# Kernel tuning notes

Hardware: AMD Instinct MI355X
Metric: run time of the kernel (lower is better)

The kernel has to match this reference:

```python
import jax, jax.numpy as jnp
import numpy as np

N = 100000
D = 128
E = 1600000


def setup_inputs() -> dict:
    key = jax.random.key(0)
    k1, k2, k3, k4 = jax.random.split(key, 4)
    x = jax.random.normal(k1, (N, D), dtype=jnp.float32)
    edge_index = jax.random.randint(k2, (2, E), 0, N, dtype=jnp.int64)
    edge_weight = jax.random.uniform(k3, (E,), dtype=jnp.float32)
    x0 = jax.random.normal(k4, (N, D), dtype=jnp.float32)
    return {
        "t": jnp.zeros((), dtype=jnp.float32),
        "x": x,
        "edge_index": edge_index,
        "edge_weight": edge_weight,
        "x0": x0,
        "alpha_train": jnp.zeros((), dtype=jnp.float32),
        "beta_train": jnp.zeros((), dtype=jnp.float32),
        "source_train": jnp.zeros((), dtype=jnp.float32),
    }


def reference(t, x, edge_index, edge_weight, x0, alpha_train, beta_train, source_train):
    # sigmoid-gated diffusion/reaction coefficients
    alpha = jax.nn.sigmoid(alpha_train) * 0.1
    beta = jax.nn.sigmoid(beta_train) * 0.1
    # sparse A @ x: out[row] += w * x[col]  (torch_sparse.spmm convention)
    row, col = edge_index[0], edge_index[1]
    msgs = x[col] * edge_weight[:, None]            # [E, D]
    ax = jax.ops.segment_sum(msgs, row, num_segments=N)  # [N, D]
    diffusion = ax - x
    reaction = -(x - 1.0) * x
    f = alpha * diffusion + beta * reaction
    source_term = jnp.clip(source_train * x0, -1.0, 1.0)
    return f + source_term * 0.1
```

## Files before the change

kernel.cpp:

```cpp
#include <hip/hip_runtime.h>
#include <math.h>


#define D_FEAT 128
#define RPB 256
#define NB_MAX 400
#define SORT_CAP 5120
#define EPB 8192

__device__ __forceinline__ float sigmoid_f(float v) {
    return 1.0f / (1.0f + __expf(-v));
}

__global__ void zero_kernel(int* __restrict__ p, int n) {
    int i = blockIdx.x * blockDim.x + threadIdx.x;
    if (i < n) p[i] = 0;
}

__global__ __launch_bounds__(256) void count_kernel(const int* __restrict__ rows,
                                                    int* __restrict__ cnt, int E, int NB) {
    __shared__ int hist[NB_MAX];
    int t = threadIdx.x;
    for (int i = t; i < NB; i += 256) hist[i] = 0;
    __syncthreads();
    int nE4 = E >> 2;
    int base4 = blockIdx.x * (EPB / 4);
#pragma unroll
    for (int k = 0; k < EPB / 4 / 256; ++k) {
        int i4 = base4 + k * 256 + t;
        if (i4 < nE4) {
            int4 r = ((const int4*)rows)[i4];
            atomicAdd(&hist[r.x >> 8], 1);
            atomicAdd(&hist[r.y >> 8], 1);
            atomicAdd(&hist[r.z >> 8], 1);
            atomicAdd(&hist[r.w >> 8], 1);
        }
    }
    if (blockIdx.x == 0 && t < (E & 3))
        atomicAdd(&hist[rows[(nE4 << 2) + t] >> 8], 1);
    __syncthreads();
    for (int i = t; i < NB; i += 256) {
        int c = hist[i];
        if (c) atomicAdd(&cnt[i], c);
    }
}

__global__ void scan_kernel(const int* __restrict__ cnt, int* __restrict__ bstart,
                            int* __restrict__ gcur, int NB) {
    int lane = threadIdx.x;
    int carry = 0;
    for (int base = 0; base < NB; base += 64) {
        int idx = base + lane;
        int v = (idx < NB) ? cnt[idx] : 0;
        int incl = v;
#pragma unroll
        for (int d = 1; d < 64; d <<= 1) {
            int tt = __shfl_up(incl, d);
            if (lane >= d) incl += tt;
        }
        int tot = __shfl(incl, 63);
        int excl = incl - v + carry;
        if (idx < NB) { bstart[idx] = excl; gcur[idx] = excl; }
        carry += tot;
    }
    if (lane == 0) bstart[NB] = carry;
}

__global__ __launch_bounds__(256) void place_kernel(const int* __restrict__ rows,
                                                    const int* __restrict__ cols,
                                                    const float* __restrict__ w,
                                                    const float* __restrict__ alpha_p,
                                                    int* __restrict__ gcur,
                                                    int2* __restrict__ raw, int E, int NB) {
    __shared__ int hist[NB_MAX];
    __shared__ int basep[NB_MAX];
    const float alpha = sigmoid_f(alpha_p[0]) * 0.1f;
    int t = threadIdx.x;
    for (int i = t; i < NB; i += 256) hist[i] = 0;
    __syncthreads();

    int base = blockIdx.x * EPB;
#pragma unroll
    for (int k = 0; k < EPB / 256; ++k) {
        int e = base + k * 256 + t;
        if (e < E) atomicAdd(&hist[rows[e] >> 8], 1);
    }
    __syncthreads();
    for (int i = t; i < NB; i += 256) {
        basep[i] = atomicAdd(&gcur[i], hist[i]);
        hist[i] = 0;
    }
    __syncthreads();
#pragma unroll
    for (int k = 0; k < EPB / 256; ++k) {
        int e = base + k * 256 + t;
        if (e >= E) continue;
        int r = rows[e];
        int bkt = r >> 8;
        int rl  = r & 255;
        int rank = atomicAdd(&hist[bkt], 1);
        raw[basep[bkt] + rank] = make_int2((rl << 17) | cols[e],
                                           __float_as_int(w[e] * alpha));
    }
}

__global__ __launch_bounds__(256) void sort_kernel(const int2* __restrict__ raw,
                                                   int2* __restrict__ srt,
                                                   const int* __restrict__ bstart,
                                                   int* __restrict__ off, int N, int NB) {
    __shared__ int2 sbuf[SORT_CAP];
    __shared__ int hist[RPB];
    __shared__ int scanb[RPB];
    __shared__ int cursor[RPB];
    int b = blockIdx.x;
    int t = threadIdx.x;
    int bs = bstart[b], be = bstart[b + 1];
    int cntb = be - bs;
    hist[t] = 0;
    __syncthreads();

    bool fast = (cntb <= SORT_CAP);
    if (fast) {
        for (int i = t; i < cntb; i += 256) {
            int2 v = raw[bs + i];
            sbuf[i] = v;
            atomicAdd(&hist[v.x >> 17], 1);
        }
    } else {
        for (int i = t; i < cntb; i += 256)
            atomicAdd(&hist[raw[bs + i].x >> 17], 1);
    }
    __syncthreads();

    int v = hist[t];
    scanb[t] = v;
    __syncthreads();
    for (int d = 1; d < 256; d <<= 1) {
        int tv = (t >= d) ? scanb[t - d] : 0;
        __syncthreads();
        scanb[t] += tv;
        __syncthreads();
    }
    int incl = scanb[t];
    int excl = incl - v;
    int row = b * RPB + t;
    if (row < N) off[row] = bs + incl;
    cursor[t] = bs + excl;
    __syncthreads();

    if (fast) {
        for (int i = t; i < cntb; i += 256) {
            int2 r = sbuf[i];
            int rl = r.x >> 17;
            int pos = atomicAdd(&cursor[rl], 1);
            srt[pos] = make_int2(r.x & 0x1FFFF, r.y);
        }
    } else {
        for (int i = t; i < cntb; i += 256) {
            int2 r = raw[bs + i];
            int rl = r.x >> 17;
            int pos = atomicAdd(&cursor[rl], 1);
            srt[pos] = make_int2(r.x & 0x1FFFF, r.y);
        }
    }
}

__global__ void gather_kernel(const float* __restrict__ x,
                              const float* __restrict__ x0,
                              const int* __restrict__ off,
                              const int2* __restrict__ col_w,
                              const float* __restrict__ alpha_p,
                              const float* __restrict__ beta_p,
                              const float* __restrict__ src_p,
                              float* __restrict__ out, int N) {
    const float alpha = sigmoid_f(alpha_p[0]) * 0.1f;
    const float beta  = sigmoid_f(beta_p[0]) * 0.1f;
    const float src   = src_p[0];

    int gtid = blockIdx.x * blockDim.x + threadIdx.x;
    int row  = gtid >> 6;
    if (row >= N) return;
    int lane  = threadIdx.x & 63;
    int half  = lane >> 5;
    int flane = lane & 31;

    int start = (row == 0) ? 0 : off[row - 1];
    int end   = off[row];

    const float4* x4 = (const float4*)x;
    float4 a0 = make_float4(0.f, 0.f, 0.f, 0.f);
    float4 a1 = make_float4(0.f, 0.f, 0.f, 0.f);

    int j = start + half;
    for (; j + 2 < end; j += 4) {
        int2 cw0 = col_w[j];
        int2 cw1 = col_w[j + 2];
        float4 v0 = x4[(long long)cw0.x * 32 + flane];
        float4 v1 = x4[(long long)cw1.x * 32 + flane];
        float w0 = __int_as_float(cw0.y);
        float w1 = __int_as_float(cw1.y);
        a0.x += w0 * v0.x; a0.y += w0 * v0.y; a0.z += w0 * v0.z; a0.w += w0 * v0.w;
        a1.x += w1 * v1.x; a1.y += w1 * v1.y; a1.z += w1 * v1.z; a1.w += w1 * v1.w;
    }
    if (j < end) {
        int2 cw = col_w[j];
        float4 v = x4[(long long)cw.x * 32 + flane];
        float wv = __int_as_float(cw.y);
        a0.x += wv * v.x; a0.y += wv * v.y; a0.z += wv * v.z; a0.w += wv * v.w;
    }
    float4 acc;
    acc.x = a0.x + a1.x; acc.y = a0.y + a1.y;
    acc.z = a0.z + a1.z; acc.w = a0.w + a1.w;

    acc.x += __shfl_xor(acc.x, 32);
    acc.y += __shfl_xor(acc.y, 32);
    acc.z += __shfl_xor(acc.z, 32);
    acc.w += __shfl_xor(acc.w, 32);

    if (half == 0) {
        long long base = (long long)row * 32 + flane;
        float4 xv  = x4[base];
        float4 x0v = ((const float4*)x0)[base];
        float xs[4]  = {xv.x, xv.y, xv.z, xv.w};
        float zs[4]  = {x0v.x, x0v.y, x0v.z, x0v.w};
        float as[4]  = {acc.x, acc.y, acc.z, acc.w};
        float os[4];
#pragma unroll
        for (int k = 0; k < 4; ++k) {
            float reaction = -(xs[k] - 1.0f) * xs[k];
            float st = fminf(fmaxf(src * zs[k], -1.0f), 1.0f);
            os[k] = as[k] - alpha * xs[k] + beta * reaction + st * 0.1f;
        }
        ((float4*)out)[base] = make_float4(os[0], os[1], os[2], os[3]);
    }
}

extern "C" void kernel_launch(void* const* d_in, const int* in_sizes, int n_in,
                              void* d_out, int out_size, void* d_ws, size_t ws_size,
                              hipStream_t stream) {
    const float* x   = (const float*)d_in[1];
    const int*   ei  = (const int*)d_in[2];
    const float* ew  = (const float*)d_in[3];
    const float* x0  = (const float*)d_in[4];
    const float* alp = (const float*)d_in[5];
    const float* bet = (const float*)d_in[6];
    const float* src = (const float*)d_in[7];
    float* out = (float*)d_out;

    const int E = in_sizes[3];
    const int N = out_size / D_FEAT;
    const int* rows = ei;
    const int* cols = ei + E;

    const int NB = (N + RPB - 1) / RPB;
    const int nEdgeBlk = (E + EPB - 1) / EPB;

    char* ws = (char*)d_ws;
    int* cnt    = (int*)ws;  ws += ((size_t)NB * 4 + 15) & ~15ull;
    int* bstart = (int*)ws;  ws += ((size_t)(NB + 1) * 4 + 15) & ~15ull;
    int* gcur   = (int*)ws;  ws += ((size_t)NB * 4 + 15) & ~15ull;
    int* off    = (int*)ws;  ws += ((size_t)N * 4 + 15) & ~15ull;
    int2* col_w = (int2*)ws; ws += ((size_t)E * 8 + 15) & ~15ull;

    int2* raw;
    if ((size_t)out_size >= (size_t)E * 8) {
        raw = (int2*)d_out;
    } else {
        raw = (int2*)ws;     ws += ((size_t)E * 8 + 15) & ~15ull;
    }

    zero_kernel<<<(NB + 255) / 256, 256, 0, stream>>>(cnt, NB);
    count_kernel<<<nEdgeBlk, 256, 0, stream>>>(rows, cnt, E, NB);
    scan_kernel<<<1, 64, 0, stream>>>(cnt, bstart, gcur, NB);
    place_kernel<<<nEdgeBlk, 256, 0, stream>>>(rows, cols, ew, alp, gcur, raw, E, NB);
    sort_kernel<<<NB, 256, 0, stream>>>(raw, col_w, bstart, off, N, NB);
    {
        long long threads = (long long)N * 64;
        int grid = (int)((threads + 255) / 256);
        gather_kernel<<<grid, 256, 0, stream>>>(x, x0, off, col_w, alp, bet, src, out, N);
    }
}
```

Measured before the change: 332.2 us.

## Halve sort bucket size, shrink place blocks, and unroll gather by four

The row buckets used by the counting sort shrink from 256 to 128 rows, which doubles the number of sort blocks and halves each block's shared staging buffer. The place kernel now handles 4096 edges per block instead of 8192, so more blocks run in parallel. The gather loop is unrolled to keep four independent row loads and accumulators in flight for more memory-level parallelism. The trade-offs are more global histogram atomics and scan entries, half the threads idle during the sort-kernel scan, and higher register pressure in gather.

```diff
diff --git a/kernel.cpp b/kernel.cpp
--- a/kernel.cpp
+++ b/kernel.cpp
@@ -3,10 +3,11 @@
 
 
 #define D_FEAT 128
-#define RPB 256
-#define NB_MAX 400
-#define SORT_CAP 5120
-#define EPB 8192
+#define RPB 128
+#define NB_MAX 800
+#define SORT_CAP 2560
+#define EPB_COUNT 8192
+#define EPB_PLACE 4096
 
 __device__ __forceinline__ float sigmoid_f(float v) {
     return 1.0f / (1.0f + __expf(-v));
@@ -24,20 +25,20 @@
     for (int i = t; i < NB; i += 256) hist[i] = 0;
     __syncthreads();
     int nE4 = E >> 2;
-    int base4 = blockIdx.x * (EPB / 4);
-#pragma unroll
-    for (int k = 0; k < EPB / 4 / 256; ++k) {
+    int base4 = blockIdx.x * (EPB_COUNT / 4);
+#pragma unroll
+    for (int k = 0; k < EPB_COUNT / 4 / 256; ++k) {
         int i4 = base4 + k * 256 + t;
         if (i4 < nE4) {
             int4 r = ((const int4*)rows)[i4];
-            atomicAdd(&hist[r.x >> 8], 1);
-            atomicAdd(&hist[r.y >> 8], 1);
-            atomicAdd(&hist[r.z >> 8], 1);
-            atomicAdd(&hist[r.w >> 8], 1);
+            atomicAdd(&hist[r.x >> 7], 1);
+            atomicAdd(&hist[r.y >> 7], 1);
+            atomicAdd(&hist[r.z >> 7], 1);
+            atomicAdd(&hist[r.w >> 7], 1);
         }
     }
     if (blockIdx.x == 0 && t < (E & 3))
-        atomicAdd(&hist[rows[(nE4 << 2) + t] >> 8], 1);
+        atomicAdd(&hist[rows[(nE4 << 2) + t] >> 7], 1);
     __syncthreads();
     for (int i = t; i < NB; i += 256) {
         int c = hist[i];
@@ -79,11 +80,11 @@
     for (int i = t; i < NB; i += 256) hist[i] = 0;
     __syncthreads();
 
-    int base = blockIdx.x * EPB;
-#pragma unroll
-    for (int k = 0; k < EPB / 256; ++k) {
+    int base = blockIdx.x * EPB_PLACE;
+#pragma unroll
+    for (int k = 0; k < EPB_PLACE / 256; ++k) {
         int e = base + k * 256 + t;
-        if (e < E) atomicAdd(&hist[rows[e] >> 8], 1);
+        if (e < E) atomicAdd(&hist[rows[e] >> 7], 1);
     }
     __syncthreads();
     for (int i = t; i < NB; i += 256) {
@@ -92,12 +93,12 @@
     }
     __syncthreads();
 #pragma unroll
-    for (int k = 0; k < EPB / 256; ++k) {
+    for (int k = 0; k < EPB_PLACE / 256; ++k) {
         int e = base + k * 256 + t;
         if (e >= E) continue;
         int r = rows[e];
-        int bkt = r >> 8;
-        int rl  = r & 255;
+        int bkt = r >> 7;
+        int rl  = r & 127;
         int rank = atomicAdd(&hist[bkt], 1);
         raw[basep[bkt] + rank] = make_int2((rl << 17) | cols[e],
                                            __float_as_int(w[e] * alpha));
@@ -116,7 +117,7 @@
     int t = threadIdx.x;
     int bs = bstart[b], be = bstart[b + 1];
     int cntb = be - bs;
-    hist[t] = 0;
+    if (t < RPB) hist[t] = 0;
     __syncthreads();
 
     bool fast = (cntb <= SORT_CAP);
@@ -132,20 +133,22 @@
     }
     __syncthreads();
 
-    int v = hist[t];
-    scanb[t] = v;
-    __syncthreads();
-    for (int d = 1; d < 256; d <<= 1) {
-        int tv = (t >= d) ? scanb[t - d] : 0;
+    int v = 0;
+    if (t < RPB) { v = hist[t]; scanb[t] = v; }
+    __syncthreads();
+    for (int d = 1; d < RPB; d <<= 1) {
+        int tv = (t >= d && t < RPB) ? scanb[t - d] : 0;
         __syncthreads();
-        scanb[t] += tv;
+        if (t < RPB) scanb[t] += tv;
         __syncthreads();
     }
-    int incl = scanb[t];
-    int excl = incl - v;
-    int row = b * RPB + t;
-    if (row < N) off[row] = bs + incl;
-    cursor[t] = bs + excl;
+    if (t < RPB) {
+        int incl = scanb[t];
+        int excl = incl - v;
+        int row = b * RPB + t;
+        if (row < N) off[row] = bs + incl;
+        cursor[t] = bs + excl;
+    }
     __syncthreads();
 
     if (fast) {
@@ -190,8 +193,28 @@
     const float4* x4 = (const float4*)x;
     float4 a0 = make_float4(0.f, 0.f, 0.f, 0.f);
     float4 a1 = make_float4(0.f, 0.f, 0.f, 0.f);
+    float4 a2 = make_float4(0.f, 0.f, 0.f, 0.f);
+    float4 a3 = make_float4(0.f, 0.f, 0.f, 0.f);
 
     int j = start + half;
+    for (; j + 6 < end; j += 8) {
+        int2 cw0 = col_w[j];
+        int2 cw1 = col_w[j + 2];
+        int2 cw2 = col_w[j + 4];
+        int2 cw3 = col_w[j + 6];
+        float4 v0 = x4[(long long)cw0.x * 32 + flane];
+        float4 v1 = x4[(long long)cw1.x * 32 + flane];
+        float4 v2 = x4[(long long)cw2.x * 32 + flane];
+        float4 v3 = x4[(long long)cw3.x * 32 + flane];
+        float w0 = __int_as_float(cw0.y);
+        float w1 = __int_as_float(cw1.y);
+        float w2 = __int_as_float(cw2.y);
+        float w3 = __int_as_float(cw3.y);
+        a0.x += w0 * v0.x; a0.y += w0 * v0.y; a0.z += w0 * v0.z; a0.w += w0 * v0.w;
+        a1.x += w1 * v1.x; a1.y += w1 * v1.y; a1.z += w1 * v1.z; a1.w += w1 * v1.w;
+        a2.x += w2 * v2.x; a2.y += w2 * v2.y; a2.z += w2 * v2.z; a2.w += w2 * v2.w;
+        a3.x += w3 * v3.x; a3.y += w3 * v3.y; a3.z += w3 * v3.z; a3.w += w3 * v3.w;
+    }
     for (; j + 2 < end; j += 4) {
         int2 cw0 = col_w[j];
         int2 cw1 = col_w[j + 2];
@@ -209,8 +232,10 @@
         a0.x += wv * v.x; a0.y += wv * v.y; a0.z += wv * v.z; a0.w += wv * v.w;
     }
     float4 acc;
-    acc.x = a0.x + a1.x; acc.y = a0.y + a1.y;
-    acc.z = a0.z + a1.z; acc.w = a0.w + a1.w;
+    acc.x = (a0.x + a1.x) + (a2.x + a3.x);
+    acc.y = (a0.y + a1.y) + (a2.y + a3.y);
+    acc.z = (a0.z + a1.z) + (a2.z + a3.z);
+    acc.w = (a0.w + a1.w) + (a2.w + a3.w);
 
     acc.x += __shfl_xor(acc.x, 32);
     acc.y += __shfl_xor(acc.y, 32);
@@ -253,7 +278,8 @@
     const int* cols = ei + E;
 
     const int NB = (N + RPB - 1) / RPB;
-    const int nEdgeBlk = (E + EPB - 1) / EPB;
+    const int nCntBlk = (E + EPB_COUNT - 1) / EPB_COUNT;
+    const int nPlcBlk = (E + EPB_PLACE - 1) / EPB_PLACE;
 
     char* ws = (char*)d_ws;
     int* cnt    = (int*)ws;  ws += ((size_t)NB * 4 + 15) & ~15ull;
@@ -270,9 +296,9 @@
     }
 
     zero_kernel<<<(NB + 255) / 256, 256, 0, stream>>>(cnt, NB);
-    count_kernel<<<nEdgeBlk, 256, 0, stream>>>(rows, cnt, E, NB);
+    count_kernel<<<nCntBlk, 256, 0, stream>>>(rows, cnt, E, NB);
     scan_kernel<<<1, 64, 0, stream>>>(cnt, bstart, gcur, NB);
-    place_kernel<<<nEdgeBlk, 256, 0, stream>>>(rows, cols, ew, alp, gcur, raw, E, NB);
+    place_kernel<<<nPlcBlk, 256, 0, stream>>>(rows, cols, ew, alp, gcur, raw, E, NB);
     sort_kernel<<<NB, 256, 0, stream>>>(raw, col_w, bstart, off, N, NB);
     {
         long long threads = (long long)N * 64;
```

After: 333.0 us. About the same (+0.2%).
